# Performance work log

Measured on AMD Instinct MI355X. Metric: run time of the kernel, lower is better.

The kernel has to match this reference:

```python
import jax, jax.numpy as jnp
import numpy as np

MIN_V, MAX_V, NORM = 0.0, 4.0, 4.0
NUM_HEADS = 8
BN_EPS = 1e-5

@jax.custom_vjp
def quant(x):
    return jnp.round(jnp.clip(x, MIN_V, MAX_V))

def _quant_fwd(x):
    return jnp.round(jnp.clip(x, MIN_V, MAX_V)), x

def _quant_bwd(x, g):
    # straight-through: zero grad outside [min, max]
    return (jnp.where((x < MIN_V) | (x > MAX_V), 0.0, g),)

quant.defvjp(_quant_fwd, _quant_bwd)

def spike(x):
    return quant(x) / NORM

def conv_bn(x, w, gamma, beta, mean, var):
    # 1x1 conv (no bias) + BatchNorm2d (eval mode, running stats)
    y = jnp.einsum('oc,bchw->bohw', w, x)
    s = gamma / jnp.sqrt(var + BN_EPS)
    return y * s[None, :, None, None] + (beta - mean * s)[None, :, None, None]


def setup_inputs() -> dict:
    key = jax.random.key(0)
    B, C, H, W = 8, 384, 64, 64
    ks = jax.random.split(key, 21)
    d = {'x': jax.random.normal(ks[0], (B, C, H, W), jnp.float32)}
    i = 1
    for p in ('q', 'k', 'v', 'p'):
        d[f'{p}_w'] = jax.random.normal(ks[i], (C, C), jnp.float32) * 0.05; i += 1
        d[f'{p}_gamma'] = jax.random.uniform(ks[i], (C,), jnp.float32, 0.5, 1.5); i += 1
        d[f'{p}_beta'] = jax.random.normal(ks[i], (C,), jnp.float32) * 0.1; i += 1
        d[f'{p}_mean'] = jax.random.normal(ks[i], (C,), jnp.float32) * 0.1; i += 1
        d[f'{p}_var'] = jax.random.uniform(ks[i], (C,), jnp.float32, 0.5, 1.5); i += 1
    return d


def reference(x, q_w, q_gamma, q_beta, q_mean, q_var,
              k_w, k_gamma, k_beta, k_mean, k_var,
              v_w, v_gamma, v_beta, v_mean, v_var,
              p_w, p_gamma, p_beta, p_mean, p_var):
    B, C, H, W = x.shape
    N = H * W
    hd = C // NUM_HEADS
    scale = hd ** -0.5

    xs = spike(x)
    q = spike(conv_bn(xs, q_w, q_gamma, q_beta, q_mean, q_var))
    k = spike(conv_bn(xs, k_w, k_gamma, k_beta, k_mean, k_var))
    v = spike(conv_bn(xs, v_w, v_gamma, v_beta, v_mean, v_var))

    # (B,C,H,W) -> (B,heads,N,hd); channel c = h*hd + d
    def to_heads(t):
        return t.reshape(B, NUM_HEADS, hd, N).transpose(0, 1, 3, 2)

    q, k, v = to_heads(q), to_heads(k), to_heads(v)

    # softmax-free attention: (q @ k^T) @ v == q @ (k^T @ v)  -> O(N*d^2)
    kv = jnp.einsum('bhnd,bhne->bhde', k, v)          # [B,H,hd,hd]
    attn = jnp.einsum('bhnd,bhde->bhne', q, kv) * (scale * 2)  # [B,H,N,hd]

    # back to (B, C_v, N): torch does transpose(2,3).reshape(B,C_v,N)
    a = attn.transpose(0, 1, 3, 2).reshape(B, C, N)
    a = spike(a).reshape(B, C, H, W)
    out = conv_bn(a, p_w, p_gamma, p_beta, p_mean, p_var)
    return out
```

## Files before the change

### kernel.cpp

```cpp
#include <hip/hip_runtime.h>
#include <stdint.h>

#define B_  8
#define C_  384
#define N_  4096
#define NH_ 8
#define HD_ 48
#define CB_ (C_*N_)
#define KS2 768

typedef __attribute__((ext_vector_type(8))) short short8;
typedef __attribute__((ext_vector_type(8))) _Float16 half8;
typedef __attribute__((ext_vector_type(4))) float f32x4;

struct P5 { const float *w, *g, *be, *mu, *va; };
struct W4 { const float *w0, *w1, *w2, *w3; };

__device__ __forceinline__ float b2f(unsigned short u) {
    union { unsigned int i; float f; } c; c.i = ((unsigned int)u) << 16; return c.f;
}
__device__ __forceinline__ unsigned short f2b(float f) {
    union { float f; unsigned int i; } c; c.f = f;
    return (unsigned short)((c.i + 0x7FFFu + ((c.i >> 16) & 1u)) >> 16);
}
__device__ __forceinline__ unsigned short f2h(float f) {
    union { _Float16 h; unsigned short u; } c; c.h = (_Float16)f; return c.u;
}
__device__ __forceinline__ float spikef(float f) {
    f = fminf(fmaxf(f, 0.0f), 4.0f);
    return rintf(f) * 0.25f;
}
__device__ __forceinline__ void async16(const void* g, void* l) {
    __builtin_amdgcn_global_load_lds((const __attribute__((address_space(1))) void*)g,
                                     (__attribute__((address_space(3))) void*)l, 16, 0, 0);
}

__global__ __launch_bounds__(256) void kprep0(const float* __restrict__ x,
                                              unsigned short* __restrict__ xst,
                                              W4 ws4, unsigned short* __restrict__ wsp) {
    int bid = blockIdx.x;
    int t = threadIdx.x;
    __shared__ __attribute__((aligned(16))) unsigned short sm[64][68];
    if (bid < 3072) {
        int nt = bid & 63, rest = bid >> 6;
        int ct = rest % 6, b = rest / 6;
        int n0 = nt * 64, c0 = ct * 64;
        const float* xb = x + (size_t)b * CB_;
        #pragma unroll
        for (int i = 0; i < 4; ++i) {
            int c = (t >> 4) + 16 * i;
            int seg = t & 15;
            float4 d = *(const float4*)(xb + (size_t)(c0 + c) * N_ + n0 + seg * 4);
            unsigned short v[4];
            v[0] = f2h(spikef(d.x)); v[1] = f2h(spikef(d.y));
            v[2] = f2h(spikef(d.z)); v[3] = f2h(spikef(d.w));
            *(uint2*)&sm[c][seg * 4] = *(const uint2*)v;
        }
        __syncthreads();
        unsigned short* ob = xst + (size_t)b * CB_;
        #pragma unroll
        for (int i = 0; i < 2; ++i) {
            int flat = i * 256 + t;
            int n = flat >> 3, segc = flat & 7;
            unsigned short v[8];
            #pragma unroll
            for (int j = 0; j < 8; ++j) v[j] = sm[segc * 8 + j][n];
            *(uint4*)(ob + (size_t)(n0 + n) * C_ + c0 + segc * 8) = *(const uint4*)v;
        }
    } else {
        int idx = (bid - 3072) * 256 + t;
        int mat = idx / 147456, rem = idx % 147456;
        int o = rem / 384, c = rem % 384;
        const float* W = (mat == 0) ? ws4.w0 : (mat == 1) ? ws4.w1 : (mat == 2) ? ws4.w2 : ws4.w3;
        float w = W[o * 384 + c];
        _Float16 hh = (fabsf(w) < 6.103515625e-05f) ? (_Float16)0 : (_Float16)w;
        float r1 = w - (float)hh;
        float s  = r1 * 4096.0f;
        union { _Float16 h; unsigned short u; } ch, cl;
        ch.h = hh; cl.h = (_Float16)s;
        unsigned short* row = wsp + (size_t)mat * 384 * KS2 + (size_t)o * KS2 + c;
        row[0] = cl.u; row[384] = ch.u;
    }
}

__global__ __launch_bounds__(256) void k1_qkv(const unsigned short* __restrict__ xst,
                                              const unsigned short* __restrict__ wsp,
                                              P5 pq, P5 pk, P5 pv,
                                              unsigned short* __restrict__ qs,
                                              unsigned short* __restrict__ ks,
                                              unsigned short* __restrict__ vs) {
    int gid = blockIdx.x;
    int xcd = gid & 7, idx = gid >> 3;
    int pairSlot = idx / 9, mt = idx - pairSlot * 9;
    int p = xcd * 32 + pairSlot;
    int ntile = p >> 3, b = p & 7;
    int mat = mt / 3;
    int orow0 = (mt % 3) * 128;
    int n0 = ntile * 128;
    int t = threadIdx.x, lane = t & 63, wvv = t >> 6;
    int wr = wvv >> 1, wc = wvv & 1;

    __shared__ __attribute__((aligned(16))) short lds[17408];
    P5 pp = (mat == 0) ? pq : (mat == 1 ? pk : pv);
    const unsigned short* abase = xst + (size_t)b * CB_;
    const unsigned short* wbase = wsp + (size_t)mat * 384 * KS2;

    f32x4 acc[4][4] = {};
    for (int kk = 0; kk < KS2; kk += 64) {
        if (kk == 384) {
            #pragma unroll
            for (int mi = 0; mi < 4; ++mi)
                #pragma unroll
                for (int ni = 0; ni < 4; ++ni)
                    acc[mi][ni] = acc[mi][ni] * 0.000244140625f;
        }
        int ck = (kk >= 384) ? kk - 384 : kk;
        #pragma unroll
        for (int j = 0; j < 4; ++j) {
            int row = wvv * 32 + j * 8 + (lane >> 3);
            int g = (lane & 7) ^ (row & 7);
            async16(abase + (size_t)(n0 + row) * C_ + ck + g * 8, lds + (wvv * 32 + j * 8) * 64);
        }
        #pragma unroll
        for (int j = 0; j < 4; ++j) {
            int row = wvv * 32 + j * 8 + (lane >> 3);
            int g = (lane & 7) ^ (row & 7);
            async16(wbase + (size_t)(orow0 + row) * KS2 + kk + g * 8, lds + 8192 + (wvv * 32 + j * 8) * 64);
        }
        __syncthreads();
        #pragma unroll
        for (int ksb = 0; ksb < 2; ++ksb) {
            half8 af[4], bfr[4];
            #pragma unroll
            for (int mi = 0; mi < 4; ++mi) {
                int row = wr * 64 + mi * 16 + (lane & 15);
                int s = (ksb * 4 + (lane >> 4)) ^ (row & 7);
                af[mi] = *(const half8*)&lds[row * 64 + s * 8];
            }
            #pragma unroll
            for (int ni = 0; ni < 4; ++ni) {
                int row = wc * 64 + ni * 16 + (lane & 15);
                int s = (ksb * 4 + (lane >> 4)) ^ (row & 7);
                bfr[ni] = *(const half8*)&lds[8192 + row * 64 + s * 8];
            }
            #pragma unroll
            for (int mi = 0; mi < 4; ++mi)
                #pragma unroll
                for (int ni = 0; ni < 4; ++ni)
                    acc[mi][ni] = __builtin_amdgcn_mfma_f32_16x16x32_f16(af[mi], bfr[ni], acc[mi][ni], 0, 0, 0);
        }
        __syncthreads();
    }

    float s_bn[4], t_bn[4];
    #pragma unroll
    for (int ni = 0; ni < 4; ++ni) {
        int o = orow0 + wc * 64 + ni * 16 + (lane & 15);
        float g = pp.g[o], be = pp.be[o], mu = pp.mu[o], va = pp.va[o];
        float s = g / sqrtf(va + 1e-5f);
        s_bn[ni] = s; t_bn[ni] = be - mu * s;
    }
    unsigned short* esm = (unsigned short*)lds;

    if (mat != 0) {
        #pragma unroll
        for (int mi = 0; mi < 4; ++mi)
            #pragma unroll
            for (int ni = 0; ni < 4; ++ni) {
                int ol = wc * 64 + ni * 16 + (lane & 15);
                int nb = wr * 64 + mi * 16 + (lane >> 4) * 4;
                unsigned short vv[4];
                #pragma unroll
                for (int r = 0; r < 4; ++r)
                    vv[r] = f2b(spikef(acc[mi][ni][r] * s_bn[ni] + t_bn[ni]));
                *(uint2*)&esm[ol * 136 + nb] = *(const uint2*)vv;
            }
        __syncthreads();
        unsigned short* dst = ((mat == 1) ? ks : vs) + (size_t)b * CB_;
        #pragma unroll
        for (int i = 0; i < 8; ++i) {
            int o = (t >> 4) + 16 * i;
            int seg = t & 15;
            uint4 d = *(const uint4*)&esm[o * 136 + seg * 8];
            *(uint4*)(dst + (size_t)(orow0 + o) * N_ + n0 + seg * 8) = d;
        }
    } else {
        #pragma unroll
        for (int mi = 0; mi < 4; ++mi)
            #pragma unroll
            for (int ni = 0; ni < 4; ++ni) {
                int ol = wc * 64 + ni * 16 + (lane & 15);
                int nb = wr * 64 + mi * 16 + (lane >> 4) * 4;
                #pragma unroll
                for (int r = 0; r < 4; ++r)
                    esm[(nb + r) * 136 + ol] = f2b(spikef(acc[mi][ni][r] * s_bn[ni] + t_bn[ni]));
            }
        __syncthreads();
        #pragma unroll
        for (int i = 0; i < 8; ++i) {
            int n = (t >> 4) + 16 * i;
            int seg = t & 15;
            uint4 d = *(const uint4*)&esm[n * 136 + seg * 8];
            *(uint4*)(qs + ((size_t)b * N_ + n0 + n) * C_ + orow0 + seg * 8) = d;
        }
    }
}

__global__ __launch_bounds__(256) void k2_kv(const unsigned short* __restrict__ ks,
                                             const unsigned short* __restrict__ vs,
                                             float* __restrict__ kvf) {
    int id = blockIdx.x;
    int b = id >> 3, h = id & 7;
    int t = threadIdx.x, lane = t & 63, w = t >> 6;
    const unsigned short* kb = ks + (size_t)b * CB_ + h * HD_ * N_;
    const unsigned short* vb = vs + (size_t)b * CB_ + h * HD_ * N_;

    f32x4 acc[3][3] = {};
    for (int kk = 0; kk < 1024; kk += 32) {
        int n = w * 1024 + kk + (lane >> 4) * 8;
        short8 af[3], bfr[3];
        #pragma unroll
        for (int di = 0; di < 3; ++di)
            af[di] = *(const short8*)(kb + (size_t)((lane & 15) + 16 * di) * N_ + n);
        #pragma unroll
        for (int ei = 0; ei < 3; ++ei)
            bfr[ei] = *(const short8*)(vb + (size_t)((lane & 15) + 16 * ei) * N_ + n);
        #pragma unroll
        for (int di = 0; di < 3; ++di)
            #pragma unroll
            for (int ei = 0; ei < 3; ++ei)
                acc[di][ei] = __builtin_amdgcn_mfma_f32_16x16x32_bf16(af[di], bfr[ei], acc[di][ei], 0, 0, 0);
    }
    __shared__ float red[4][48][48];
    #pragma unroll
    for (int di = 0; di < 3; ++di)
        #pragma unroll
        for (int ei = 0; ei < 3; ++ei) {
            int d0 = di * 16 + (lane >> 4) * 4;
            int e = ei * 16 + (lane & 15);
            #pragma unroll
            for (int r = 0; r < 4; ++r) red[w][d0 + r][e] = acc[di][ei][r];
        }
    __syncthreads();
    float* dst = kvf + (size_t)(b * NH_ + h) * 2304;
    for (int i = t; i < 2304; i += 256) {
        int e = i / 48, d = i % 48;
        dst[e * 48 + d] = red[0][d][e] + red[1][d][e] + red[2][d][e] + red[3][d][e];
    }
}

__global__ __launch_bounds__(256) void k3_attn(const unsigned short* __restrict__ qs,
                                               const float* __restrict__ kvf,
                                               unsigned short* __restrict__ as_) {
    int id = blockIdx.x;
    int hg = id & 1, nt = (id >> 1) & 63, b = id >> 7;
    int t = threadIdx.x, lane = t & 63, w = t >> 6;
    int nb0 = nt * 64;
    __shared__ __attribute__((aligned(16))) unsigned short ldsq[64 * 24 * 8];
    __shared__ __attribute__((aligned(16))) unsigned short ldsh[48 * 72];
    __shared__ __attribute__((aligned(16))) unsigned short ldsl[48 * 72];

    const unsigned short* qb = qs + ((size_t)b * N_ + nb0) * C_ + hg * 192;
    #pragma unroll
    for (int i = 0; i < 6; ++i) {
        int g = (i * 4 + w) * 64;
        int f = g + lane;
        int row = f / 24, sc = f % 24;
        int c = sc ^ (row & 7);
        async16(qb + (size_t)row * C_ + c * 8, ldsq + (size_t)g * 8);
    }
    const float* kvb = kvf + ((size_t)(b * NH_ + hg * 4)) * 2304;
    const float S2 = 0.28867513459481287f;
    int quad = lane >> 4;
    int qrow = w * 16 + (lane & 15);

    for (int hl = 0; hl < 4; ++hl) {
        __syncthreads();
        const float* kvh = kvb + hl * 2304;
        for (int i = t; i < 48 * 64; i += 256) {
            int e = i >> 6, d = i & 63;
            unsigned short h16 = 0, l16 = 0;
            if (d < 48) {
                float v = kvh[e * 48 + d];
                h16 = f2b(v);
                l16 = f2b(v - b2f(h16));
            }
            ldsh[e * 72 + d] = h16;
            ldsl[e * 72 + d] = l16;
        }
        __syncthreads();

        f32x4 acc[3] = {};
        #pragma unroll
        for (int ksb = 0; ksb < 2; ++ksb) {
            int c = hl * 6 + ksb * 4 + quad;
            int cc = c > 23 ? 23 : c;
            int slot = cc ^ (qrow & 7);
            short8 a = *(const short8*)&ldsq[(qrow * 24 + slot) * 8];
            #pragma unroll
            for (int ei = 0; ei < 3; ++ei) {
                int e = ei * 16 + (lane & 15);
                short8 bh = *(const short8*)&ldsh[e * 72 + ksb * 32 + quad * 8];
                short8 bl = *(const short8*)&ldsl[e * 72 + ksb * 32 + quad * 8];
                acc[ei] = __builtin_amdgcn_mfma_f32_16x16x32_bf16(a, bh, acc[ei], 0, 0, 0);
                acc[ei] = __builtin_amdgcn_mfma_f32_16x16x32_bf16(a, bl, acc[ei], 0, 0, 0);
            }
        }
        #pragma unroll
        for (int ei = 0; ei < 3; ++ei) {
            int col = hl * 48 + ei * 16 + (lane & 15);
            int ch = col >> 3, j = col & 7;
            #pragma unroll
            for (int r = 0; r < 4; ++r) {
                int row = w * 16 + quad * 4 + r;
                ldsq[(row * 24 + (ch ^ (row & 7))) * 8 + j] = f2h(spikef(acc[ei][r] * S2));
            }
        }
    }
    __syncthreads();
    unsigned short* ob = as_ + ((size_t)b * N_ + nb0) * C_ + hg * 192;
    #pragma unroll
    for (int i = 0; i < 6; ++i) {
        int f = i * 256 + t;
        int row = f / 24, sc = f % 24;
        int slot = sc ^ (row & 7);
        uint4 d = *(const uint4*)&ldsq[(row * 24 + slot) * 8];
        *(uint4*)(ob + (size_t)row * C_ + sc * 8) = d;
    }
}

__global__ __launch_bounds__(256) void k4_pconv(const unsigned short* __restrict__ as_,
                                                const unsigned short* __restrict__ wsp,
                                                P5 pp,
                                                float* __restrict__ out) {
    int gid = blockIdx.x;
    int xcd = gid & 7, idx = gid >> 3;
    int pairSlot = idx / 3, mt = idx - pairSlot * 3;
    int p = xcd * 32 + pairSlot;
    int ntile = p >> 3, b = p & 7;
    int orow0 = mt * 128;
    int n0 = ntile * 128;
    int t = threadIdx.x, lane = t & 63, wvv = t >> 6;
    int wr = wvv >> 1, wc = wvv & 1;

    __shared__ __attribute__((aligned(16))) char ldsb[33792];
    short* lds = (short*)ldsb;
    const unsigned short* abase = as_ + (size_t)b * CB_;
    const unsigned short* wbase = wsp + (size_t)3 * 384 * KS2;

    f32x4 acc[4][4] = {};
    for (int kk = 0; kk < KS2; kk += 64) {
        if (kk == 384) {
            #pragma unroll
            for (int mi = 0; mi < 4; ++mi)
                #pragma unroll
                for (int ni = 0; ni < 4; ++ni)
                    acc[mi][ni] = acc[mi][ni] * 0.000244140625f;
        }
        int ck = (kk >= 384) ? kk - 384 : kk;
        #pragma unroll
        for (int j = 0; j < 4; ++j) {
            int row = wvv * 32 + j * 8 + (lane >> 3);
            int g = (lane & 7) ^ (row & 7);
            async16(abase + (size_t)(n0 + row) * C_ + ck + g * 8, lds + (wvv * 32 + j * 8) * 64);
        }
        #pragma unroll
        for (int j = 0; j < 4; ++j) {
            int row = wvv * 32 + j * 8 + (lane >> 3);
            int g = (lane & 7) ^ (row & 7);
            async16(wbase + (size_t)(orow0 + row) * KS2 + kk + g * 8, lds + 8192 + (wvv * 32 + j * 8) * 64);
        }
        __syncthreads();
        #pragma unroll
        for (int ksb = 0; ksb < 2; ++ksb) {
            half8 af[4], bfr[4];
            #pragma unroll
            for (int mi = 0; mi < 4; ++mi) {
                int row = wr * 64 + mi * 16 + (lane & 15);
                int s = (ksb * 4 + (lane >> 4)) ^ (row & 7);
                af[mi] = *(const half8*)&lds[row * 64 + s * 8];
            }
            #pragma unroll
            for (int ni = 0; ni < 4; ++ni) {
                int row = wc * 64 + ni * 16 + (lane & 15);
                int s = (ksb * 4 + (lane >> 4)) ^ (row & 7);
                bfr[ni] = *(const half8*)&lds[8192 + row * 64 + s * 8];
            }
            #pragma unroll
            for (int mi = 0; mi < 4; ++mi)
                #pragma unroll
                for (int ni = 0; ni < 4; ++ni)
                    acc[mi][ni] = __builtin_amdgcn_mfma_f32_16x16x32_f16(af[mi], bfr[ni], acc[mi][ni], 0, 0, 0);
        }
        __syncthreads();
    }

    float s_bn[4], t_bn[4];
    #pragma unroll
    for (int ni = 0; ni < 4; ++ni) {
        int o = orow0 + wc * 64 + ni * 16 + (lane & 15);
        float g = pp.g[o], be = pp.be[o], mu = pp.mu[o], va = pp.va[o];
        float s = g / sqrtf(va + 1e-5f);
        s_bn[ni] = s; t_bn[ni] = be - mu * s;
    }
    float* fsm = (float*)ldsb;
    for (int half = 0; half < 2; ++half) {
        __syncthreads();
        if (wc == half) {
            #pragma unroll
            for (int mi = 0; mi < 4; ++mi)
                #pragma unroll
                for (int ni = 0; ni < 4; ++ni) {
                    int ol = ni * 16 + (lane & 15);
                    int nl = wr * 64 + mi * 16 + (lane >> 4) * 4;
                    f32x4 vv;
                    #pragma unroll
                    for (int r = 0; r < 4; ++r)
                        vv[r] = acc[mi][ni][r] * s_bn[ni] + t_bn[ni];
                    *(f32x4*)&fsm[ol * 132 + nl] = vv;
                }
        }
        __syncthreads();
        #pragma unroll
        for (int i = 0; i < 8; ++i) {
            int f = i * 256 + t;
            int o = f >> 5, slot = f & 31;
            f32x4 vv = *(const f32x4*)&fsm[o * 132 + slot * 4];
            *(f32x4*)(out + ((size_t)b * C_ + orow0 + half * 64 + o) * N_ + n0 + slot * 4) = vv;
        }
    }
}

extern "C" void kernel_launch(void* const* d_in, const int* in_sizes, int n_in,
                              void* d_out, int out_size, void* d_ws, size_t ws_size,
                              hipStream_t stream) {
    P5 pq { (const float*)d_in[1],  (const float*)d_in[2],  (const float*)d_in[3],
            (const float*)d_in[4],  (const float*)d_in[5] };
    P5 pk { (const float*)d_in[6],  (const float*)d_in[7],  (const float*)d_in[8],
            (const float*)d_in[9],  (const float*)d_in[10] };
    P5 pv { (const float*)d_in[11], (const float*)d_in[12], (const float*)d_in[13],
            (const float*)d_in[14], (const float*)d_in[15] };
    P5 pp { (const float*)d_in[16], (const float*)d_in[17], (const float*)d_in[18],
            (const float*)d_in[19], (const float*)d_in[20] };
    W4 w4 { pq.w, pk.w, pv.w, pp.w };

    char* ws = (char*)d_ws;
    const size_t S = (size_t)B_ * C_ * N_ * 2;
    unsigned short* xst = (unsigned short*)ws;
    unsigned short* qs  = (unsigned short*)(ws + S);
    unsigned short* ks  = (unsigned short*)(ws + 2 * S + 256);
    unsigned short* vs  = (unsigned short*)(ws + 3 * S + 512);
    float*          kvf = (float*)(ws + 4 * S + 768);
    unsigned short* wsp = (unsigned short*)(ws + 4 * S + 768 + 589824);
    unsigned short* as_ = xst;

    kprep0<<<5376, 256, 0, stream>>>((const float*)d_in[0], xst, w4, wsp);
    k1_qkv<<<2304, 256, 0, stream>>>(xst, wsp, pq, pk, pv, qs, ks, vs);
    k2_kv<<<64, 256, 0, stream>>>(ks, vs, kvf);
    k3_attn<<<1024, 256, 0, stream>>>(qs, kvf, as_);
    k4_pconv<<<768, 256, 0, stream>>>(as_, wsp, pp, (float*)d_out);
}
```

Baseline: 268.8 us.

## Split k2 KV reduction across four N-quarters and enlarge prep transpose tiles

The K^T·V kernel now launches 256 blocks instead of 64, each covering a quarter of the sequence. It writes partial 48x48 sums, and the attention kernel adds the four partials when it loads KV. This is meant to fix the low occupancy of k2, which had only 64 blocks on a GPU with many more CUs. The x spike/transpose prep now handles 256-column tiles per block, giving fewer, larger blocks with more work each. The cost is extra partial-sum traffic and redundant summation in each k3 block.

```diff
diff --git a/kernel.cpp b/kernel.cpp
--- a/kernel.cpp
+++ b/kernel.cpp
@@ -40,35 +40,35 @@
                                               W4 ws4, unsigned short* __restrict__ wsp) {
     int bid = blockIdx.x;
     int t = threadIdx.x;
-    __shared__ __attribute__((aligned(16))) unsigned short sm[64][68];
-    if (bid < 3072) {
-        int nt = bid & 63, rest = bid >> 6;
+    __shared__ __attribute__((aligned(16))) unsigned short sm[64 * 260];
+    if (bid < 768) {
+        int n16 = bid & 15, rest = bid >> 4;
         int ct = rest % 6, b = rest / 6;
-        int n0 = nt * 64, c0 = ct * 64;
+        int n0 = n16 * 256, c0 = ct * 64;
+        int w = t >> 6, l = t & 63;
         const float* xb = x + (size_t)b * CB_;
         #pragma unroll
-        for (int i = 0; i < 4; ++i) {
-            int c = (t >> 4) + 16 * i;
-            int seg = t & 15;
-            float4 d = *(const float4*)(xb + (size_t)(c0 + c) * N_ + n0 + seg * 4);
+        for (int it = 0; it < 16; ++it) {
+            int r = it * 4 + w;
+            float4 d = *(const float4*)(xb + (size_t)(c0 + r) * N_ + n0 + l * 4);
             unsigned short v[4];
             v[0] = f2h(spikef(d.x)); v[1] = f2h(spikef(d.y));
             v[2] = f2h(spikef(d.z)); v[3] = f2h(spikef(d.w));
-            *(uint2*)&sm[c][seg * 4] = *(const uint2*)v;
+            *(uint2*)&sm[r * 260 + l * 4] = *(const uint2*)v;
         }
         __syncthreads();
         unsigned short* ob = xst + (size_t)b * CB_;
         #pragma unroll
-        for (int i = 0; i < 2; ++i) {
-            int flat = i * 256 + t;
-            int n = flat >> 3, segc = flat & 7;
+        for (int it = 0; it < 8; ++it) {
+            int f = it * 256 + t;
+            int n = f >> 3, cs = f & 7;
             unsigned short v[8];
             #pragma unroll
-            for (int j = 0; j < 8; ++j) v[j] = sm[segc * 8 + j][n];
-            *(uint4*)(ob + (size_t)(n0 + n) * C_ + c0 + segc * 8) = *(const uint4*)v;
+            for (int j = 0; j < 8; ++j) v[j] = sm[(cs * 8 + j) * 260 + n];
+            *(uint4*)(ob + (size_t)(n0 + n) * C_ + c0 + cs * 8) = *(const uint4*)v;
         }
     } else {
-        int idx = (bid - 3072) * 256 + t;
+        int idx = (bid - 768) * 256 + t;
         int mat = idx / 147456, rem = idx % 147456;
         int o = rem / 384, c = rem % 384;
         const float* W = (mat == 0) ? ws4.w0 : (mat == 1) ? ws4.w1 : (mat == 2) ? ws4.w2 : ws4.w3;
@@ -208,16 +208,17 @@
 
 __global__ __launch_bounds__(256) void k2_kv(const unsigned short* __restrict__ ks,
                                              const unsigned short* __restrict__ vs,
-                                             float* __restrict__ kvf) {
+                                             float* __restrict__ kvp) {
     int id = blockIdx.x;
-    int b = id >> 3, h = id & 7;
+    int b = id >> 5, h = (id >> 2) & 7, q4 = id & 3;
     int t = threadIdx.x, lane = t & 63, w = t >> 6;
     const unsigned short* kb = ks + (size_t)b * CB_ + h * HD_ * N_;
     const unsigned short* vb = vs + (size_t)b * CB_ + h * HD_ * N_;
+    int nbase = q4 * 1024 + w * 256;
 
     f32x4 acc[3][3] = {};
-    for (int kk = 0; kk < 1024; kk += 32) {
-        int n = w * 1024 + kk + (lane >> 4) * 8;
+    for (int kk = 0; kk < 256; kk += 32) {
+        int n = nbase + kk + (lane >> 4) * 8;
         short8 af[3], bfr[3];
         #pragma unroll
         for (int di = 0; di < 3; ++di)
@@ -242,7 +243,7 @@
             for (int r = 0; r < 4; ++r) red[w][d0 + r][e] = acc[di][ei][r];
         }
     __syncthreads();
-    float* dst = kvf + (size_t)(b * NH_ + h) * 2304;
+    float* dst = kvp + ((size_t)(b * NH_ + h) * 4 + q4) * 2304;
     for (int i = t; i < 2304; i += 256) {
         int e = i / 48, d = i % 48;
         dst[e * 48 + d] = red[0][d][e] + red[1][d][e] + red[2][d][e] + red[3][d][e];
@@ -250,7 +251,7 @@
 }
 
 __global__ __launch_bounds__(256) void k3_attn(const unsigned short* __restrict__ qs,
-                                               const float* __restrict__ kvf,
+                                               const float* __restrict__ kvp,
                                                unsigned short* __restrict__ as_) {
     int id = blockIdx.x;
     int hg = id & 1, nt = (id >> 1) & 63, b = id >> 7;
@@ -269,19 +270,19 @@
         int c = sc ^ (row & 7);
         async16(qb + (size_t)row * C_ + c * 8, ldsq + (size_t)g * 8);
     }
-    const float* kvb = kvf + ((size_t)(b * NH_ + hg * 4)) * 2304;
     const float S2 = 0.28867513459481287f;
     int quad = lane >> 4;
     int qrow = w * 16 + (lane & 15);
 
     for (int hl = 0; hl < 4; ++hl) {
         __syncthreads();
-        const float* kvh = kvb + hl * 2304;
+        const float* kvh = kvp + (size_t)((b * NH_ + hg * 4 + hl) * 4) * 2304;
         for (int i = t; i < 48 * 64; i += 256) {
             int e = i >> 6, d = i & 63;
             unsigned short h16 = 0, l16 = 0;
             if (d < 48) {
-                float v = kvh[e * 48 + d];
+                int o = e * 48 + d;
+                float v = kvh[o] + kvh[2304 + o] + kvh[4608 + o] + kvh[6912 + o];
                 h16 = f2b(v);
                 l16 = f2b(v - b2f(h16));
             }
@@ -450,13 +451,13 @@
     unsigned short* qs  = (unsigned short*)(ws + S);
     unsigned short* ks  = (unsigned short*)(ws + 2 * S + 256);
     unsigned short* vs  = (unsigned short*)(ws + 3 * S + 512);
-    float*          kvf = (float*)(ws + 4 * S + 768);
-    unsigned short* wsp = (unsigned short*)(ws + 4 * S + 768 + 589824);
+    float*          kvp = (float*)(ws + 4 * S + 768);
+    unsigned short* wsp = (unsigned short*)(ws + 4 * S + 768 + 2359296);
     unsigned short* as_ = xst;
 
-    kprep0<<<5376, 256, 0, stream>>>((const float*)d_in[0], xst, w4, wsp);
+    kprep0<<<3072, 256, 0, stream>>>((const float*)d_in[0], xst, w4, wsp);
     k1_qkv<<<2304, 256, 0, stream>>>(xst, wsp, pq, pk, pv, qs, ks, vs);
-    k2_kv<<<64, 256, 0, stream>>>(ks, vs, kvf);
-    k3_attn<<<1024, 256, 0, stream>>>(qs, kvf, as_);
+    k2_kv<<<256, 256, 0, stream>>>(ks, vs, kvp);
+    k3_attn<<<1024, 256, 0, stream>>>(qs, kvp, as_);
     k4_pconv<<<768, 256, 0, stream>>>(as_, wsp, pp, (float*)d_out);
 }
```

After: 263.9 us. No clear change (-1.8%).
